# Kernel tuning notes

Hardware: AMD Instinct MI355X
Metric: run time of the kernel (lower is better)

## Reference

```python
import jax, jax.numpy as jnp
import numpy as np

B, T, C = 4, 2048, 1024
H = 16
D = C // H  # head_size = 64


def setup_inputs() -> dict:
    key = jax.random.key(0)
    ks = jax.random.split(key, 6)
    s = 0.02
    x = jax.random.normal(ks[0], (B, T, C), dtype=jnp.float32)
    # per-head projections (bias=False), stacked over heads: [H, C, D]
    Wq = jax.random.normal(ks[1], (H, C, D), dtype=jnp.float32) * s
    Wk = jax.random.normal(ks[2], (H, C, D), dtype=jnp.float32) * s
    Wv = jax.random.normal(ks[3], (H, C, D), dtype=jnp.float32) * s
    # output projection Linear(H*D, C)
    Wo = jax.random.normal(ks[4], (H * D, C), dtype=jnp.float32) * s
    bo = jax.random.normal(ks[5], (C,), dtype=jnp.float32) * s
    return {"x": x, "Wq": Wq, "Wk": Wk, "Wv": Wv, "Wo": Wo, "bo": bo}


def reference(x, Wq, Wk, Wv, Wo, bo):
    # q,k,v: [B, H, T, D]
    q = jnp.einsum('btc,hcd->bhtd', x, Wq)
    k = jnp.einsum('btc,hcd->bhtd', x, Wk)
    v = jnp.einsum('btc,hcd->bhtd', x, Wv)
    scale = 1.0 / jnp.sqrt(jnp.asarray(D, dtype=x.dtype))
    scores = jnp.einsum('bhtd,bhsd->bhts', q, k) * scale  # [B,H,T,T]
    causal = jnp.tril(jnp.ones((T, T), dtype=bool))
    scores = jnp.where(causal, scores, jnp.asarray(-jnp.inf, dtype=scores.dtype))
    wei = jax.nn.softmax(scores, axis=-1)
    out = jnp.einsum('bhts,bhsd->bhtd', wei, v)  # [B,H,T,D]
    # concat heads along last dim (head order = module list order)
    out = jnp.transpose(out, (0, 2, 1, 3)).reshape(B, T, H * D)
    return out @ Wo + bo
```

## Files before the change

kernel.cpp:

```cpp
#include <hip/hip_runtime.h>
#include <math.h>

typedef __attribute__((ext_vector_type(8))) short short8;
typedef __attribute__((ext_vector_type(4))) short short4v;
typedef __attribute__((ext_vector_type(4))) float floatx4;

#define AS1 __attribute__((address_space(1)))
#define AS3 __attribute__((address_space(3)))

__device__ inline void gload_lds16(const short* g, short* l) {
    __builtin_amdgcn_global_load_lds((const AS1 unsigned int*)g,
                                     (AS3 unsigned int*)l, 16, 0, 0);
}

__device__ inline short f2bf(float f) {
    unsigned u = __builtin_bit_cast(unsigned, f);
    u += 0x7fffu + ((u >> 16) & 1u);
    return (short)(u >> 16);
}

__global__ __launch_bounds__(256) void conv_x(
    const float* __restrict__ x, short* __restrict__ xb)
{
    int i = (blockIdx.x * 256 + threadIdx.x) * 4;
    float4 v = *(const float4*)&x[i];
    short4v o = { f2bf(v.x), f2bf(v.y), f2bf(v.z), f2bf(v.w) };
    *(short4v*)&xb[i] = o;
}

__global__ __launch_bounds__(256) void transpose_w(
    const float* __restrict__ Wq, const float* __restrict__ Wk,
    const float* __restrict__ Wv, const float* __restrict__ Wo,
    short* __restrict__ Wall, short* __restrict__ WoT)
{
    __shared__ short T[64 * 72];
    const int kt = blockIdx.x, y = blockIdx.y;
    const int tid = threadIdx.x;
    const int lr = tid >> 2, lc = (tid & 3) * 16;
    #pragma unroll 1
    for (int m = 0; m < 4; ++m) {
        const float* src;
        float s = 1.f;
        if (m < 3) {
            const float* W = (m == 0) ? Wq : (m == 1) ? Wk : Wv;
            src = W + ((size_t)y << 16) + (size_t)(kt * 64 + lr) * 64 + lc;
            if (m == 0) s = 0.125f * 1.44269504088896f;
        } else {
            src = Wo + (size_t)(kt * 64 + lr) * 1024 + y * 64 + lc;
        }
        short8 t0, t1;
        {
            float4 v0 = *(const float4*)(src + 0);
            float4 v1 = *(const float4*)(src + 4);
            float4 v2 = *(const float4*)(src + 8);
            float4 v3 = *(const float4*)(src + 12);
            t0[0]=f2bf(v0.x*s); t0[1]=f2bf(v0.y*s); t0[2]=f2bf(v0.z*s); t0[3]=f2bf(v0.w*s);
            t0[4]=f2bf(v1.x*s); t0[5]=f2bf(v1.y*s); t0[6]=f2bf(v1.z*s); t0[7]=f2bf(v1.w*s);
            t1[0]=f2bf(v2.x*s); t1[1]=f2bf(v2.y*s); t1[2]=f2bf(v2.z*s); t1[3]=f2bf(v2.w*s);
            t1[4]=f2bf(v3.x*s); t1[5]=f2bf(v3.y*s); t1[6]=f2bf(v3.z*s); t1[7]=f2bf(v3.w*s);
        }
        *(short8*)&T[lr * 72 + lc]     = t0;
        *(short8*)&T[lr * 72 + lc + 8] = t1;
        __syncthreads();
        short8 o0, o1;
        #pragma unroll
        for (int j = 0; j < 8; ++j) o0[j] = T[(lc + j) * 72 + lr];
        #pragma unroll
        for (int j = 0; j < 8; ++j) o1[j] = T[(lc + 8 + j) * 72 + lr];
        short* dst = (m < 3)
            ? Wall + (size_t)(m * 1024 + y * 64 + lr) * 1024 + kt * 64
            : WoT  + (size_t)(y * 64 + lr) * 1024 + kt * 64;
        *(short8*)&dst[lc]     = o0;
        *(short8*)&dst[lc + 8] = o1;
        __syncthreads();
    }
}

__global__ __launch_bounds__(256) void transpose_v(
    const short* __restrict__ Vp, short* __restrict__ Vt_g)
{
    __shared__ short T[64 * 72];
    const int t0 = blockIdx.x * 64;
    const int h = blockIdx.y, b = blockIdx.z;
    const int tid = threadIdx.x;
    const int r = tid >> 3, c = (tid & 7) * 8;
    #pragma unroll
    for (int p = 0; p < 2; ++p) {
        int t = r + 32 * p;
        *(short8*)&T[t * 72 + c] =
            *(const short8*)&Vp[(size_t)(b * 2048 + t0 + t) * 1024 + h * 64 + c];
    }
    __syncthreads();
    const int d = tid >> 2, tc = (tid & 3) * 16;
    size_t obase = ((size_t)(b * 16 + h)) * 64 * 2048 + (size_t)d * 2048 + t0 + tc;
    short8 o0, o1;
    #pragma unroll
    for (int j = 0; j < 8; ++j) o0[j] = T[(tc + j) * 72 + d];
    #pragma unroll
    for (int j = 0; j < 8; ++j) o1[j] = T[(tc + 8 + j) * 72 + d];
    *(short8*)&Vt_g[obase] = o0;
    *(short8*)&Vt_g[obase + 8] = o1;
}

__global__ __launch_bounds__(256) void gemm_bt(
    const short* __restrict__ A, const short* __restrict__ BT,
    short* __restrict__ C, short* __restrict__ Cv, float* __restrict__ Cf,
    const float* __restrict__ bias, int M, int N, int K, int split)
{
    __shared__ short As[128 * 32];
    __shared__ short Bs[128 * 32];
    const int tid  = threadIdx.x;
    const int wid  = tid >> 6, lane = tid & 63;
    const int quad = lane >> 4, l15 = lane & 15;
    const int m0 = blockIdx.x * 128, n0 = blockIdx.y * 128;
    const int wr = (wid >> 1) * 64, wc = (wid & 1) * 64;

    floatx4 acc[4][4] = {};

    const int srow = wid * 32 + (lane >> 2);
    const int scol = (lane & 3) * 8;

    for (int k0 = 0; k0 < K; k0 += 32) {
        #pragma unroll
        for (int t = 0; t < 2; ++t) {
            gload_lds16(A  + (size_t)(m0 + srow + t * 16) * K + k0 + scol,
                        &As[(wid * 32 + t * 16) * 32]);
            gload_lds16(BT + (size_t)(n0 + srow + t * 16) * K + k0 + scol,
                        &Bs[(wid * 32 + t * 16) * 32]);
        }
        __syncthreads();
        short8 bfr[4];
        #pragma unroll
        for (int j = 0; j < 4; ++j)
            bfr[j] = *(const short8*)&Bs[(wc + j * 16 + l15) * 32 + quad * 8];
        #pragma unroll
        for (int i = 0; i < 4; ++i) {
            short8 afr = *(const short8*)&As[(wr + i * 16 + l15) * 32 + quad * 8];
            #pragma unroll
            for (int j = 0; j < 4; ++j)
                acc[i][j] = __builtin_amdgcn_mfma_f32_16x16x32_bf16(
                    afr, bfr[j], acc[i][j], 0, 0, 0);
        }
        __syncthreads();
    }

    #pragma unroll
    for (int i = 0; i < 4; ++i) {
        int row = m0 + wr + i * 16 + quad * 4;
        #pragma unroll
        for (int j = 0; j < 4; ++j) {
            int col = n0 + wc + j * 16 + l15;
            if (Cf) {
                float bv = bias ? bias[col] : 0.f;
                #pragma unroll
                for (int r = 0; r < 4; ++r)
                    Cf[(size_t)(row + r) * N + col] = acc[i][j][r] + bv;
            } else if (split) {
                int plane = col >> 10, c1 = col & 1023;
                short* dst = (plane == 2) ? Cv
                           : C + (size_t)plane * 8192 * 1024;
                #pragma unroll
                for (int r = 0; r < 4; ++r)
                    dst[(size_t)(row + r) * 1024 + c1] = f2bf(acc[i][j][r]);
            } else {
                #pragma unroll
                for (int r = 0; r < 4; ++r)
                    C[(size_t)(row + r) * 1024 + col] = f2bf(acc[i][j][r]);
            }
        }
    }
}

__global__ __launch_bounds__(256) void attn_fwd(
    const short* __restrict__ Q, const short* __restrict__ Kg,
    const short* __restrict__ Vt_g, short* __restrict__ O)
{
    __shared__ short Ks[2][64 * 72];
    __shared__ short Vs[2][64 * 72];
    __shared__ short Pb[4 * 32 * 72];
    const int tid  = threadIdx.x;
    const int wid  = tid >> 6, lane = tid & 63;
    const int quad = lane >> 4, l15 = lane & 15;
    const int pi = blockIdx.x, h = blockIdx.y, b = blockIdx.z;
    const size_t base  = ((size_t)b * 2048) * 1024 + h * 64;
    const size_t vbase = ((size_t)(b * 16 + h)) * 64 * 2048;
    const int sr = tid >> 3, sc = (tid & 7) * 8;
    short* Pw = &Pb[wid * 32 * 72];

    const short one_bf = (short)0x3F80;
    const short8 bones = { one_bf, one_bf, one_bf, one_bf,
                           one_bf, one_bf, one_bf, one_bf };

    for (int ph = 0; ph < 2; ++ph) {
        const int qt = ph ? pi : 15 - pi;
        short8 qf[2][2];
        #pragma unroll
        for (int mt = 0; mt < 2; ++mt)
            #pragma unroll
            for (int ks = 0; ks < 2; ++ks)
                qf[mt][ks] = *(const short8*)&Q[base +
                    (size_t)(qt * 128 + wid * 32 + mt * 16 + l15) * 1024 + ks * 32 + quad * 8];

        floatx4 oacc[2][4] = {};
        floatx4 lacc[2] = {};
        const int dst = 2 * qt + (wid >> 1);
        const int nst = 2 * qt + 2;

        const short* kcur = Kg + base + (size_t)sr * 1024 + sc;
        const short* vcur = Vt_g + vbase + (size_t)sr * 2048 + sc;

        short8 kv[2], vv[2];
        #pragma unroll
        for (int p = 0; p < 2; ++p) {
            kv[p] = *(const short8*)(kcur + (size_t)p * 32 * 1024);
            vv[p] = *(const short8*)(vcur + (size_t)p * 32 * 2048);
        }
        kcur += 64 * 1024; vcur += 64;
        #pragma unroll
        for (int p = 0; p < 2; ++p) {
            int row = sr + 32 * p;
            *(short8*)&Ks[0][row * 72 + sc] = kv[p];
            *(short8*)&Vs[0][row * 72 + sc] = vv[p];
        }
        #pragma unroll
        for (int p = 0; p < 2; ++p) {
            kv[p] = *(const short8*)(kcur + (size_t)p * 32 * 1024);
            vv[p] = *(const short8*)(vcur + (size_t)p * 32 * 2048);
        }
        kcur += 64 * 1024; vcur += 64;
        __syncthreads();

        for (int st = 0; st < nst; ++st) {
            const short* K0 = Ks[st & 1];
            const short* V0 = Vs[st & 1];
            if (st + 1 < nst) {
                short* K1 = Ks[(st + 1) & 1];
                short* V1 = Vs[(st + 1) & 1];
                #pragma unroll
                for (int p = 0; p < 2; ++p) {
                    int row = sr + 32 * p;
                    *(short8*)&K1[row * 72 + sc] = kv[p];
                    *(short8*)&V1[row * 72 + sc] = vv[p];
                }
            }
            if (st + 2 < nst) {
                #pragma unroll
                for (int p = 0; p < 2; ++p) {
                    kv[p] = *(const short8*)(kcur + (size_t)p * 32 * 1024);
                    vv[p] = *(const short8*)(vcur + (size_t)p * 32 * 2048);
                }
                kcur += 64 * 1024; vcur += 64;
            }

            if (st <= dst) {
                floatx4 sf[2][4];
                #pragma unroll
                for (int nt = 0; nt < 4; ++nt) {
                    floatx4 z0 = {}, z1 = {};
                    #pragma unroll
                    for (int ks = 0; ks < 2; ++ks) {
                        short8 bfr = *(const short8*)&K0[(nt * 16 + l15) * 72 + ks * 32 + quad * 8];
                        z0 = __builtin_amdgcn_mfma_f32_16x16x32_bf16(qf[0][ks], bfr, z0, 0, 0, 0);
                        z1 = __builtin_amdgcn_mfma_f32_16x16x32_bf16(qf[1][ks], bfr, z1, 0, 0, 0);
                    }
                    sf[0][nt] = z0; sf[1][nt] = z1;
                }

                if (st == dst) {
                    #pragma unroll
                    for (int mt = 0; mt < 2; ++mt)
                        #pragma unroll
                        for (int nt = 0; nt < 4; ++nt)
                            #pragma unroll
                            for (int r = 0; r < 4; ++r) {
                                int qa = qt * 128 + wid * 32 + mt * 16 + quad * 4 + r;
                                int sa = st * 64 + nt * 16 + l15;
                                if (sa > qa) sf[mt][nt][r] = -INFINITY;
                            }
                }

                #pragma unroll
                for (int mt = 0; mt < 2; ++mt)
                    #pragma unroll
                    for (int nt = 0; nt < 4; ++nt)
                        #pragma unroll
                        for (int r = 0; r < 4; ++r) {
                            float p = __builtin_amdgcn_exp2f(sf[mt][nt][r]);
                            unsigned u = __builtin_bit_cast(unsigned, p) + 0x8000u;
                            Pw[(mt * 16 + quad * 4 + r) * 72 + ((nt ^ quad) * 16) + l15] =
                                (short)(u >> 16);
                        }

                #pragma unroll
                for (int ks = 0; ks < 2; ++ks) {
                    int blk = (ks * 2 + (quad >> 1)) ^ (l15 >> 2);
                    short8 af0 = *(const short8*)&Pw[(l15) * 72 + blk * 16 + (quad & 1) * 8];
                    short8 af1 = *(const short8*)&Pw[(16 + l15) * 72 + blk * 16 + (quad & 1) * 8];
                    lacc[0] = __builtin_amdgcn_mfma_f32_16x16x32_bf16(af0, bones, lacc[0], 0, 0, 0);
                    lacc[1] = __builtin_amdgcn_mfma_f32_16x16x32_bf16(af1, bones, lacc[1], 0, 0, 0);
                    #pragma unroll
                    for (int nt = 0; nt < 4; ++nt) {
                        short8 bfr = *(const short8*)&V0[(nt * 16 + l15) * 72 + ks * 32 + quad * 8];
                        oacc[0][nt] = __builtin_amdgcn_mfma_f32_16x16x32_bf16(af0, bfr, oacc[0][nt], 0, 0, 0);
                        oacc[1][nt] = __builtin_amdgcn_mfma_f32_16x16x32_bf16(af1, bfr, oacc[1][nt], 0, 0, 0);
                    }
                }
            }
            __syncthreads();
        }

        #pragma unroll
        for (int mt = 0; mt < 2; ++mt)
            #pragma unroll
            for (int nt = 0; nt < 4; ++nt)
                #pragma unroll
                for (int r = 0; r < 4; ++r) {
                    float v = oacc[mt][nt][r] / lacc[mt][r];
                    int qa = qt * 128 + wid * 32 + mt * 16 + quad * 4 + r;
                    O[base + (size_t)qa * 1024 + nt * 16 + l15] = f2bf(v);
                }
    }
}

extern "C" void kernel_launch(void* const* d_in, const int* in_sizes, int n_in,
                              void* d_out, int out_size, void* d_ws, size_t ws_size,
                              hipStream_t stream) {
    const float* x  = (const float*)d_in[0];
    const float* Wq = (const float*)d_in[1];
    const float* Wk = (const float*)d_in[2];
    const float* Wv = (const float*)d_in[3];
    const float* Wo = (const float*)d_in[4];
    const float* bo = (const float*)d_in[5];
    float* out = (float*)d_out;

    char* ws = (char*)d_ws;
    const size_t MB = 1024 * 1024;
    short* xb   = (short*)(ws + 0 * MB);
    short* Vt_g = (short*)(ws + 0 * MB);
    short* Vr   = (short*)(ws + 16 * MB);
    short* Ao   = (short*)(ws + 16 * MB);
    short* Wall = (short*)(ws + 32 * MB);
    short* WoT  = (short*)(ws + 38 * MB);
    short* Qp   = (short*)d_out;
    short* Kp   = Qp + 8 * 1024 * 1024;

    conv_x<<<8192, 256, 0, stream>>>(x, xb);
    transpose_w<<<dim3(16, 16), 256, 0, stream>>>(Wq, Wk, Wv, Wo, Wall, WoT);

    gemm_bt<<<dim3(64, 24), 256, 0, stream>>>(xb, Wall, Qp, Vr, nullptr, nullptr,
                                              8192, 3072, 1024, 1);
    transpose_v<<<dim3(32, 16, 4), 256, 0, stream>>>(Vr, Vt_g);

    attn_fwd<<<dim3(8, 16, 4), 256, 0, stream>>>(Qp, Kp, Vt_g, Ao);

    gemm_bt<<<dim3(64, 8), 256, 0, stream>>>(Ao, WoT, nullptr, nullptr, out, bo,
                                             8192, 1024, 1024, 0);
}
```

Measured before the change: 287.4 us.

## Use direct global-to-LDS loads with XOR swizzle in attention, split output GEMM

The attention kernel now streams K and V tiles straight into LDS with global_load_lds, replacing the register-staged loads and stores. The unpadded 64-wide tiles use an XOR swizzle to avoid bank conflicts, which cuts VGPR pressure and LDS store instructions. The output projection gets its own gemm_o kernel with 64x128 tiles, doubling the block count to 1024 for better CU occupancy. Bf16 rounding of P is also changed from round-half-up to truncation, which saves an add but adds a small bias.

After: 280.0 us. -2.6%, faster.

```diff
diff --git a/kernel.cpp b/kernel.cpp
--- a/kernel.cpp
+++ b/kernel.cpp
@@ -104,8 +104,7 @@
 
 __global__ __launch_bounds__(256) void gemm_bt(
     const short* __restrict__ A, const short* __restrict__ BT,
-    short* __restrict__ C, short* __restrict__ Cv, float* __restrict__ Cf,
-    const float* __restrict__ bias, int M, int N, int K, int split)
+    short* __restrict__ C, short* __restrict__ Cv, int M, int N, int K)
 {
     __shared__ short As[128 * 32];
     __shared__ short Bs[128 * 32];
@@ -150,23 +149,64 @@
         #pragma unroll
         for (int j = 0; j < 4; ++j) {
             int col = n0 + wc + j * 16 + l15;
-            if (Cf) {
-                float bv = bias ? bias[col] : 0.f;
-                #pragma unroll
-                for (int r = 0; r < 4; ++r)
-                    Cf[(size_t)(row + r) * N + col] = acc[i][j][r] + bv;
-            } else if (split) {
-                int plane = col >> 10, c1 = col & 1023;
-                short* dst = (plane == 2) ? Cv
-                           : C + (size_t)plane * 8192 * 1024;
-                #pragma unroll
-                for (int r = 0; r < 4; ++r)
-                    dst[(size_t)(row + r) * 1024 + c1] = f2bf(acc[i][j][r]);
-            } else {
-                #pragma unroll
-                for (int r = 0; r < 4; ++r)
-                    C[(size_t)(row + r) * 1024 + col] = f2bf(acc[i][j][r]);
-            }
+            int plane = col >> 10, c1 = col & 1023;
+            short* dst = (plane == 2) ? Cv : C + (size_t)plane * 8192 * 1024;
+            #pragma unroll
+            for (int r = 0; r < 4; ++r)
+                dst[(size_t)(row + r) * 1024 + c1] = f2bf(acc[i][j][r]);
+        }
+    }
+}
+
+__global__ __launch_bounds__(256) void gemm_o(
+    const short* __restrict__ A, const short* __restrict__ BT,
+    float* __restrict__ Cf, const float* __restrict__ bias, int N, int K)
+{
+    __shared__ short As[64 * 32];
+    __shared__ short Bs[128 * 32];
+    const int tid  = threadIdx.x;
+    const int wid  = tid >> 6, lane = tid & 63;
+    const int quad = lane >> 4, l15 = lane & 15;
+    const int m0 = blockIdx.x * 64, n0 = blockIdx.y * 128;
+    const int wr = (wid >> 1) * 32, wc = (wid & 1) * 64;
+
+    floatx4 acc[2][4] = {};
+
+    const int arow = tid >> 2, acol = (tid & 3) * 8;
+    const int brow = wid * 32 + (lane >> 2), bcol = (lane & 3) * 8;
+
+    for (int k0 = 0; k0 < K; k0 += 32) {
+        gload_lds16(A + (size_t)(m0 + arow) * K + k0 + acol, &As[(wid * 16) * 32]);
+        #pragma unroll
+        for (int t = 0; t < 2; ++t)
+            gload_lds16(BT + (size_t)(n0 + brow + t * 16) * K + k0 + bcol,
+                        &Bs[(wid * 32 + t * 16) * 32]);
+        __syncthreads();
+        short8 bfr[4];
+        #pragma unroll
+        for (int j = 0; j < 4; ++j)
+            bfr[j] = *(const short8*)&Bs[(wc + j * 16 + l15) * 32 + quad * 8];
+        #pragma unroll
+        for (int i = 0; i < 2; ++i) {
+            short8 afr = *(const short8*)&As[(wr + i * 16 + l15) * 32 + quad * 8];
+            #pragma unroll
+            for (int j = 0; j < 4; ++j)
+                acc[i][j] = __builtin_amdgcn_mfma_f32_16x16x32_bf16(
+                    afr, bfr[j], acc[i][j], 0, 0, 0);
+        }
+        __syncthreads();
+    }
+
+    #pragma unroll
+    for (int i = 0; i < 2; ++i) {
+        int row = m0 + wr + i * 16 + quad * 4;
+        #pragma unroll
+        for (int j = 0; j < 4; ++j) {
+            int col = n0 + wc + j * 16 + l15;
+            float bv = bias[col];
+            #pragma unroll
+            for (int r = 0; r < 4; ++r)
+                Cf[(size_t)(row + r) * N + col] = acc[i][j][r] + bv;
         }
     }
 }
@@ -175,8 +215,8 @@
     const short* __restrict__ Q, const short* __restrict__ Kg,
     const short* __restrict__ Vt_g, short* __restrict__ O)
 {
-    __shared__ short Ks[2][64 * 72];
-    __shared__ short Vs[2][64 * 72];
+    __shared__ short Ks[2][64 * 64];
+    __shared__ short Vs[2][64 * 64];
     __shared__ short Pb[4 * 32 * 72];
     const int tid  = threadIdx.x;
     const int wid  = tid >> 6, lane = tid & 63;
@@ -184,8 +224,13 @@
     const int pi = blockIdx.x, h = blockIdx.y, b = blockIdx.z;
     const size_t base  = ((size_t)b * 2048) * 1024 + h * 64;
     const size_t vbase = ((size_t)(b * 16 + h)) * 64 * 2048;
-    const int sr = tid >> 3, sc = (tid & 7) * 8;
     short* Pw = &Pb[wid * 32 * 72];
+
+    const int srow = tid >> 3;
+    const int gcol = ((tid & 7) ^ (srow & 7)) * 8;
+    const int lbase0 = (wid * 8) * 64;
+    const int lbase1 = (wid * 8 + 32) * 64;
+    const int l7 = l15 & 7;
 
     const short one_bf = (short)0x3F80;
     const short8 bones = { one_bf, one_bf, one_bf, one_bf,
@@ -206,28 +251,14 @@
         const int dst = 2 * qt + (wid >> 1);
         const int nst = 2 * qt + 2;
 
-        const short* kcur = Kg + base + (size_t)sr * 1024 + sc;
-        const short* vcur = Vt_g + vbase + (size_t)sr * 2048 + sc;
-
-        short8 kv[2], vv[2];
-        #pragma unroll
-        for (int p = 0; p < 2; ++p) {
-            kv[p] = *(const short8*)(kcur + (size_t)p * 32 * 1024);
-            vv[p] = *(const short8*)(vcur + (size_t)p * 32 * 2048);
-        }
-        kcur += 64 * 1024; vcur += 64;
-        #pragma unroll
-        for (int p = 0; p < 2; ++p) {
-            int row = sr + 32 * p;
-            *(short8*)&Ks[0][row * 72 + sc] = kv[p];
-            *(short8*)&Vs[0][row * 72 + sc] = vv[p];
-        }
-        #pragma unroll
-        for (int p = 0; p < 2; ++p) {
-            kv[p] = *(const short8*)(kcur + (size_t)p * 32 * 1024);
-            vv[p] = *(const short8*)(vcur + (size_t)p * 32 * 2048);
-        }
-        kcur += 64 * 1024; vcur += 64;
+        const short* kptr = Kg + base + (size_t)srow * 1024 + gcol;
+        const short* vptr = Vt_g + vbase + (size_t)srow * 2048 + gcol;
+
+        gload_lds16(kptr,               &Ks[0][lbase0]);
+        gload_lds16(kptr + 32 * 1024,   &Ks[0][lbase1]);
+        gload_lds16(vptr,               &Vs[0][lbase0]);
+        gload_lds16(vptr + 32 * 2048,   &Vs[0][lbase1]);
+        kptr += 64 * 1024; vptr += 64;
         __syncthreads();
 
         for (int st = 0; st < nst; ++st) {
@@ -236,20 +267,11 @@
             if (st + 1 < nst) {
                 short* K1 = Ks[(st + 1) & 1];
                 short* V1 = Vs[(st + 1) & 1];
-                #pragma unroll
-                for (int p = 0; p < 2; ++p) {
-                    int row = sr + 32 * p;
-                    *(short8*)&K1[row * 72 + sc] = kv[p];
-                    *(short8*)&V1[row * 72 + sc] = vv[p];
-                }
-            }
-            if (st + 2 < nst) {
-                #pragma unroll
-                for (int p = 0; p < 2; ++p) {
-                    kv[p] = *(const short8*)(kcur + (size_t)p * 32 * 1024);
-                    vv[p] = *(const short8*)(vcur + (size_t)p * 32 * 2048);
-                }
-                kcur += 64 * 1024; vcur += 64;
+                gload_lds16(kptr,             &K1[lbase0]);
+                gload_lds16(kptr + 32 * 1024, &K1[lbase1]);
+                gload_lds16(vptr,             &V1[lbase0]);
+                gload_lds16(vptr + 32 * 2048, &V1[lbase1]);
+                kptr += 64 * 1024; vptr += 64;
             }
 
             if (st <= dst) {
@@ -259,7 +281,8 @@
                     floatx4 z0 = {}, z1 = {};
                     #pragma unroll
                     for (int ks = 0; ks < 2; ++ks) {
-                        short8 bfr = *(const short8*)&K0[(nt * 16 + l15) * 72 + ks * 32 + quad * 8];
+                        short8 bfr = *(const short8*)&K0[(nt * 16 + l15) * 64 +
+                                                         (((ks * 4 + quad) ^ l7) * 8)];
                         z0 = __builtin_amdgcn_mfma_f32_16x16x32_bf16(qf[0][ks], bfr, z0, 0, 0, 0);
                         z1 = __builtin_amdgcn_mfma_f32_16x16x32_bf16(qf[1][ks], bfr, z1, 0, 0, 0);
                     }
@@ -286,7 +309,7 @@
                         #pragma unroll
                         for (int r = 0; r < 4; ++r) {
                             float p = __builtin_amdgcn_exp2f(sf[mt][nt][r]);
-                            unsigned u = __builtin_bit_cast(unsigned, p) + 0x8000u;
+                            unsigned u = __builtin_bit_cast(unsigned, p);
                             Pw[(mt * 16 + quad * 4 + r) * 72 + ((nt ^ quad) * 16) + l15] =
                                 (short)(u >> 16);
                         }
@@ -300,7 +323,8 @@
                     lacc[1] = __builtin_amdgcn_mfma_f32_16x16x32_bf16(af1, bones, lacc[1], 0, 0, 0);
                     #pragma unroll
                     for (int nt = 0; nt < 4; ++nt) {
-                        short8 bfr = *(const short8*)&V0[(nt * 16 + l15) * 72 + ks * 32 + quad * 8];
+                        short8 bfr = *(const short8*)&V0[(nt * 16 + l15) * 64 +
+                                                         (((ks * 4 + quad) ^ l7) * 8)];
                         oacc[0][nt] = __builtin_amdgcn_mfma_f32_16x16x32_bf16(af0, bfr, oacc[0][nt], 0, 0, 0);
                         oacc[1][nt] = __builtin_amdgcn_mfma_f32_16x16x32_bf16(af1, bfr, oacc[1][nt], 0, 0, 0);
                     }
@@ -347,12 +371,10 @@
     conv_x<<<8192, 256, 0, stream>>>(x, xb);
     transpose_w<<<dim3(16, 16), 256, 0, stream>>>(Wq, Wk, Wv, Wo, Wall, WoT);
 
-    gemm_bt<<<dim3(64, 24), 256, 0, stream>>>(xb, Wall, Qp, Vr, nullptr, nullptr,
-                                              8192, 3072, 1024, 1);
+    gemm_bt<<<dim3(64, 24), 256, 0, stream>>>(xb, Wall, Qp, Vr, 8192, 3072, 1024);
     transpose_v<<<dim3(32, 16, 4), 256, 0, stream>>>(Vr, Vt_g);
 
     attn_fwd<<<dim3(8, 16, 4), 256, 0, stream>>>(Qp, Kp, Vt_g, Ao);
 
-    gemm_bt<<<dim3(64, 8), 256, 0, stream>>>(Ao, WoT, nullptr, nullptr, out, bo,
-                                             8192, 1024, 1024, 0);
-}
+    gemm_o<<<dim3(128, 8), 256, 0, stream>>>(Ao, WoT, out, bo, 1024, 1024);
+}
```
